# Performance work log

Measured on AMD Instinct MI355X. Metric: run time of the kernel, lower is better.

The kernel has to match this reference:

```python
import jax, jax.numpy as jnp
import numpy as np

B, N, T = 8, 128, 1024
D, LD, H, NQ = 512, 64, 8, 3
HD = D // H
Q = 1 + NQ


def _layernorm(h, g, b):
    m = jnp.mean(h, axis=-1, keepdims=True)
    v = jnp.var(h, axis=-1, keepdims=True)
    return (h - m) * jax.lax.rsqrt(v + 1e-5) * g + b


def setup_inputs() -> dict:
    key = jax.random.key(0)
    ks = jax.random.split(key, 24)
    s = 0.02
    # monotone one-hot alignment: each frame assigned to a sorted phoneme index
    idx = jnp.sort(jax.random.randint(ks[0], (B, T), 0, N), axis=1)
    alignments = jax.nn.one_hot(idx, N, dtype=jnp.float32)  # [B,T,N]
    return dict(
        embeddings=jax.random.normal(ks[1], (B, N, D), jnp.float32),
        alignments=alignments,
        x=jax.random.normal(ks[2], (B, T, D), jnp.float32),
        padding_mask_phoneme=jnp.zeros((B, N), bool),
        padding_mask_frames=jnp.zeros((B, T), bool),
        kl_loss_pooler_weight=jnp.float32(0.01),
        eps=jax.random.normal(ks[3], (B, N, LD), jnp.float32),
        learnable_queries=jax.random.normal(ks[4], (1, 1, NQ, D), jnp.float32),
        in_proj_w=jax.random.normal(ks[5], (3 * D, D), jnp.float32) * s,
        in_proj_b=jnp.zeros((3 * D,), jnp.float32),
        out_proj_w=jax.random.normal(ks[6], (D, D), jnp.float32) * s,
        out_proj_b=jnp.zeros((D,), jnp.float32),
        ln_g=jnp.ones((D,), jnp.float32),
        ln_b=jnp.zeros((D,), jnp.float32),
        bot_w=jax.random.normal(ks[7], (D, Q * D), jnp.float32) * s,
        bot_b=jnp.zeros((D,), jnp.float32),
        mu_w=jax.random.normal(ks[8], (LD, D), jnp.float32) * s,
        mu_b=jnp.zeros((LD,), jnp.float32),
        lv_w=jax.random.normal(ks[9], (LD, D), jnp.float32) * s,
        lv_b=jnp.zeros((LD,), jnp.float32),
        conv1_w=jax.random.normal(ks[10], (D, LD + 1, 3), jnp.float32) * s,
        conv1_b=jnp.zeros((D,), jnp.float32),
        conv2_w=jax.random.normal(ks[11], (D, D, 3), jnp.float32) * s,
        conv2_b=jnp.zeros((D,), jnp.float32),
    )


def reference(embeddings, alignments, x, padding_mask_phoneme, padding_mask_frames,
              kl_loss_pooler_weight, eps, learnable_queries, in_proj_w, in_proj_b,
              out_proj_w, out_proj_b, ln_g, ln_b, bot_w, bot_b, mu_w, mu_b,
              lv_w, lv_b, conv1_w, conv1_b, conv2_w, conv2_b):
    b, n, d = embeddings.shape
    t = x.shape[1]
    # queries: per-phoneme embedding + learnable queries -> [B, N*Q, D]
    q_learn = jnp.broadcast_to(learnable_queries, (b, n, NQ, d))
    queries = jnp.concatenate([embeddings[:, :, None, :], q_learn], axis=2).reshape(b, n * Q, d)
    # data-dependent attention mask from alignments: True = masked
    m = jnp.transpose(alignments, (0, 2, 1))[:, :, None, :]        # [B,N,1,T]
    bool_mask = jnp.broadcast_to(m, (b, n, Q, t)).reshape(b, n * Q, t) == 0
    all_true = jnp.all(bool_mask, axis=-1, keepdims=True)
    bool_mask = jnp.where(all_true, False, bool_mask)
    # multihead cross-attention
    wq, wk, wv = jnp.split(in_proj_w, 3)
    bq, bk, bv = jnp.split(in_proj_b, 3)
    q = (queries @ wq.T + bq).reshape(b, n * Q, H, HD)
    k = (x @ wk.T + bk).reshape(b, t, H, HD)
    v = (x @ wv.T + bv).reshape(b, t, H, HD)
    scores = jnp.einsum('blhd,bshd->bhls', q, k) / jnp.sqrt(jnp.float32(HD))
    scores = jnp.where(bool_mask[:, None, :, :], -jnp.inf, scores)
    attn = jax.nn.softmax(scores, axis=-1)
    ctx = jnp.einsum('bhls,bshd->blhd', attn, v).reshape(b, n * Q, d)
    attn_out = ctx @ out_proj_w.T + out_proj_b
    qn = _layernorm(queries + attn_out, ln_g, ln_b).reshape(b, n, Q * d)
    hidden = jax.nn.silu(qn @ bot_w.T + bot_b)
    # duration-based pooling of x onto phonemes
    dur = jnp.sum(alignments, axis=1)[:, :, None]                  # [B,N,1]
    hidden = hidden + jnp.einsum('btn,btd->bnd', alignments, x) / (dur + 1e-8)
    mu_z = hidden @ mu_w.T + mu_b
    logvar_z = hidden @ lv_w.T + lv_b
    z = mu_z + eps * jnp.exp(0.5 * logvar_z)
    # upsample back to frames + phase feature
    z_up = jnp.einsum('btn,bnl->btl', alignments, z)               # [B,T,LD]
    dur2 = jnp.clip(jnp.sum(alignments, axis=1), 1e-5)             # [B,N]
    running = jnp.cumsum(alignments, axis=1) - 0.5
    phase = jnp.sum((running / dur2[:, None, :]) * alignments, axis=-1, keepdims=True)
    zc = jnp.transpose(jnp.concatenate([z_up, phase], axis=-1), (0, 2, 1))  # [B,LD+1,T]
    dn = ('NCH', 'OIH', 'NCH')
    y = jax.lax.conv_general_dilated(zc, conv1_w, (1,), 'SAME', dimension_numbers=dn) + conv1_b[None, :, None]
    y = jax.nn.silu(y)
    y = jax.lax.conv_general_dilated(y, conv2_w, (1,), 'SAME', dimension_numbers=dn) + conv2_b[None, :, None]
    x_recon = jnp.transpose(y, (0, 2, 1))                          # [B,T,D]
    # losses (masked-select replaced with jit-friendly masked sums)
    valid_p = (~padding_mask_phoneme)[..., None].astype(mu_z.dtype)
    kl = -0.5 * jnp.sum((1.0 + logvar_z - mu_z ** 2 - jnp.exp(logvar_z)) * valid_p)
    kl = kl * jnp.reshape(kl_loss_pooler_weight, ())
    valid_f = (~padding_mask_frames)[..., None].astype(x.dtype)
    diff = (x - x_recon) * valid_f
    cnt = jnp.sum(valid_f) * d
    l1 = jnp.sum(jnp.abs(diff)) / cnt
    l2 = jnp.sum(diff ** 2) / cnt
    return x_recon, kl, l1 + l2
```

## Files before the change

kernel.cpp:

```cpp
#include <hip/hip_runtime.h>
#include <hip/hip_bf16.h>
#include <math.h>

#define B_  8
#define N_  128
#define T_  1024
#define D_  512
#define LD_ 64
#define H_  8
#define Q_  4

typedef __hip_bfloat16 bf16;
typedef __attribute__((ext_vector_type(8))) short short8v;
typedef __attribute__((ext_vector_type(4))) float f32x4;
typedef __attribute__((ext_vector_type(4))) float float4v;
typedef __attribute__((ext_vector_type(4))) unsigned int uint4v;

__device__ __forceinline__ void gload16(const void* g, void* l) {
  __builtin_amdgcn_global_load_lds(
      (const __attribute__((address_space(1))) void*)g,
      (__attribute__((address_space(3))) void*)l, 16, 0, 0);
}

__device__ __forceinline__ void f2b4s(const float* in, bf16* out) {
  float4v v = *(const float4v*)in;
  bf16 o[4] = {bf16(v.x), bf16(v.y), bf16(v.z), bf16(v.w)};
  *(ulong1*)out = *(ulong1*)o;
}

__global__ __launch_bounds__(256) void k_prep(
    const float* __restrict__ x, const float* __restrict__ inw,
    const float* __restrict__ outw, const float* __restrict__ botw,
    const float* __restrict__ c1w, const float* __restrict__ c2w,
    const float* __restrict__ emb, const float* __restrict__ lq,
    bf16* __restrict__ xb, bf16* __restrict__ inwb, bf16* __restrict__ outwb,
    bf16* __restrict__ botwb, bf16* __restrict__ w1tb, bf16* __restrict__ w2tb,
    bf16* __restrict__ qryB,
    int* __restrict__ dur, int* __restrict__ segst, float* __restrict__ lacc)
{
  int g = blockIdx.x * 256 + threadIdx.x;
  if (g < 1048576) {
    f2b4s(x + (size_t)g * 4, xb + (size_t)g * 4);
  } else if (g < 1245184) {
    int i = g - 1048576;
    f2b4s(inw + (size_t)i * 4, inwb + (size_t)i * 4);
  } else if (g < 1310720) {
    int i = g - 1245184;
    f2b4s(outw + (size_t)i * 4, outwb + (size_t)i * 4);
  } else if (g < 1572864) {
    int i = g - 1310720;
    f2b4s(botw + (size_t)i * 4, botwb + (size_t)i * 4);
  } else if (g < 1703936) {
    int i = g - 1572864;
    int kk = i & 255, c = i >> 8;
    float v = 0.f;
    if (kk < 195) { int tap = kk / 65, ii = kk - tap * 65; v = c1w[c * 195 + ii * 3 + tap]; }
    w1tb[i] = bf16(v);
  } else if (g < 2490368) {
    int i = g - 1703936;
    int kk = i % 1536, co = i / 1536;
    int tap = kk >> 9, ci = kk & 511;
    w2tb[i] = bf16(c2w[co * 1536 + ci * 3 + tap]);
  } else if (g < 3014656) {
    int i4 = g - 2490368;
    int e = i4 * 4;
    int d = e & 511;
    int row = e >> 9;
    int j = row & 3;
    int bn = row >> 2;
    const float* src = (j == 0) ? emb + (size_t)bn * 512 + d
                                : lq + (size_t)(j - 1) * 512 + d;
    f2b4s(src, qryB + (size_t)e);
  } else if (g < 3015680) {
    int i = g - 3014656;
    dur[i] = 0; segst[i] = 0x7fffffff;
  } else if (g < 3015682) {
    lacc[g - 3015680] = 0.f;
  }
}

__global__ __launch_bounds__(256) void k_seg_build(
    const float* __restrict__ align, int* __restrict__ idx,
    int* __restrict__ dur, int* __restrict__ segst) {
  int row = blockIdx.x * 4 + (threadIdx.x >> 6);
  int lane = threadIdx.x & 63;
  const float* r = align + (size_t)row * N_;
  unsigned long long m0 = __ballot(r[lane] > 0.5f);
  unsigned long long m1 = __ballot(r[lane + 64] > 0.5f);
  if (lane == 0) {
    int n = m0 ? (__ffsll(m0) - 1) : (m1 ? (__ffsll(m1) - 1 + 64) : 0);
    idx[row] = n;
    int b = row >> 10, t = row & 1023;
    atomicAdd(&dur[b * N_ + n], 1);
    atomicMin(&segst[b * N_ + n], t);
  }
}

template<int EPI, int APAD, int CMODE, typename CT>
__global__ __launch_bounds__(256, 2) void k_mgemm(
    const bf16* __restrict__ A, int lda,
    const bf16* __restrict__ W, int ldw,
    const float* __restrict__ bias,
    CT* __restrict__ C, int ldc,
    int M, int Nc, int K,
    const float* __restrict__ xref = nullptr,
    float* __restrict__ lacc = nullptr)
{
  __shared__ __align__(16) short As[3][4096];
  __shared__ __align__(16) short Bs[3][8192];
  const int tid = threadIdx.x;
  const int m0 = blockIdx.y * 64;
  const int n0 = blockIdx.x * 128;
  const int kbase = blockIdx.z * K;
  const int w = tid >> 6, lane = tid & 63;
  const int wn = w * 32;
  const int lr = lane & 15;
  const int cg = lane >> 4;

  const int rg = lane >> 3;
  const int soff = (((lane & 7) ^ rg) << 3);
  const int rA = w * 8 + rg;
  int gA0 = m0 + rA, gA1 = m0 + rA + 32;
  int ar0 = APAD ? gA0 + ((gA0 >> 10) << 1) : gA0;
  int ar1 = APAD ? gA1 + ((gA1 >> 10) << 1) : gA1;
  const size_t aOff0 = (size_t)ar0 * lda + kbase + soff;
  const size_t aOff1 = (size_t)ar1 * lda + kbase + soff;
  size_t wOffs[4];
#pragma unroll
  for (int j = 0; j < 4; ++j)
    wOffs[j] = (size_t)(n0 + rA + j * 32) * ldw + kbase + soff;

  const int nt = K >> 6;

#define STAGE_(tt, buf) do { \
    size_t kk_ = (size_t)(tt) * 64; \
    gload16(A + aOff0 + kk_, &As[buf][tid * 8]); \
    gload16(A + aOff1 + kk_, &As[buf][2048 + tid * 8]); \
    gload16(W + wOffs[0] + kk_, &Bs[buf][tid * 8]); \
    gload16(W + wOffs[1] + kk_, &Bs[buf][2048 + tid * 8]); \
    gload16(W + wOffs[2] + kk_, &Bs[buf][4096 + tid * 8]); \
    gload16(W + wOffs[3] + kk_, &Bs[buf][6144 + tid * 8]); \
  } while (0)

  STAGE_(0, 0);
  if (nt > 1) STAGE_(1, 1);

  f32x4 acc[4][2] = {};
  int cur = 0;
  for (int t = 0; t < nt; ++t) {
    if (t + 2 < nt) {
      int b2 = cur + 2; if (b2 >= 3) b2 -= 3;
      STAGE_(t + 2, b2);
      asm volatile("s_waitcnt vmcnt(12)" ::: "memory");
    } else if (t + 1 < nt) {
      asm volatile("s_waitcnt vmcnt(6)" ::: "memory");
    } else {
      asm volatile("s_waitcnt vmcnt(0)" ::: "memory");
    }
    __builtin_amdgcn_sched_barrier(0);
    __builtin_amdgcn_s_barrier();
    __builtin_amdgcn_sched_barrier(0);
#pragma unroll
    for (int h = 0; h < 2; ++h) {
      short8v af[4], bfv[2];
#pragma unroll
      for (int i = 0; i < 4; ++i) {
        int rr = i * 16 + lr;
        af[i] = *(const short8v*)&As[cur][rr * 64 + (((h * 4 + cg) ^ (rr & 7)) << 3)];
      }
#pragma unroll
      for (int j = 0; j < 2; ++j) {
        int rr = wn + j * 16 + lr;
        bfv[j] = *(const short8v*)&Bs[cur][rr * 64 + (((h * 4 + cg) ^ (rr & 7)) << 3)];
      }
      __builtin_amdgcn_s_setprio(1);
#pragma unroll
      for (int i = 0; i < 4; ++i)
#pragma unroll
        for (int j = 0; j < 2; ++j)
          acc[i][j] = __builtin_amdgcn_mfma_f32_16x16x32_bf16(af[i], bfv[j], acc[i][j], 0, 0, 0);
      __builtin_amdgcn_s_setprio(0);
    }
    __builtin_amdgcn_sched_barrier(0);
    __builtin_amdgcn_s_barrier();
    __builtin_amdgcn_sched_barrier(0);
    cur = (cur == 2) ? 0 : cur + 1;
  }
#undef STAGE_

  if (EPI == 3) C += (size_t)blockIdx.z * M * ldc;
  const int orow = (lane >> 4) * 4;
  const int ocol = lane & 15;
  float la = 0.f, lb = 0.f;
#pragma unroll
  for (int i = 0; i < 4; ++i) {
#pragma unroll
    for (int q = 0; q < 4; ++q) {
      int gm = m0 + i * 16 + orow + q;
      int cr = CMODE ? gm + ((gm >> 10) << 1) + 1 : gm;
#pragma unroll
      for (int j = 0; j < 2; ++j) {
        int gn = n0 + wn + j * 16 + ocol;
        float v = acc[i][j][q];
        if (EPI != 3) v += bias[gn];
        if (EPI == 1) v = v / (1.f + __expf(-v));
        if (EPI == 4) {
          float diff = xref[(size_t)gm * Nc + gn] - v;
          la += fabsf(diff);
          lb += diff * diff;
        }
        C[(size_t)cr * ldc + gn] = (CT)v;
      }
    }
  }
  if (EPI == 4) {
    __shared__ float sh1[4], sh2[4];
#pragma unroll
    for (int off = 32; off; off >>= 1) { la += __shfl_xor(la, off); lb += __shfl_xor(lb, off); }
    if (lane == 0) { sh1[w] = la; sh2[w] = lb; }
    __syncthreads();
    if (tid == 0) {
      atomicAdd(&lacc[0], sh1[0] + sh1[1] + sh1[2] + sh1[3]);
      atomicAdd(&lacc[1], sh2[0] + sh2[1] + sh2[2] + sh2[3]);
    }
  }
}

__global__ __launch_bounds__(256) void k_attn(
    const bf16* __restrict__ qbuf, const bf16* __restrict__ kv,
    const int* __restrict__ segst, const int* __restrict__ dur,
    bf16* __restrict__ ctx)
{
  int bn = blockIdx.x;
  int b = bn >> 7;
  int w = threadIdx.x >> 6;
  int lane = threadIdx.x & 63;
  int s0 = segst[bn], cnt = dur[bn];
  if (cnt == 0) { s0 = 0; cnt = T_; }
  size_t qrow = (size_t)bn * 4 + w;
  const bf16* kvb = kv + ((size_t)b * T_ + s0) * 1024;

  float qf[8];
  {
    uint4v qv = *(const uint4v*)(qbuf + qrow * 512 + lane * 8);
#pragma unroll
    for (int i = 0; i < 4; ++i) {
      unsigned u = qv[i];
      qf[2 * i]     = __uint_as_float(u << 16);
      qf[2 * i + 1] = __uint_as_float(u & 0xffff0000u);
    }
  }

  float m = -1e30f, l = 0.f;
  float o[8] = {};
  for (int s = 0; s < cnt; s += 4) {
    float sc4[4];
#pragma unroll
    for (int u = 0; u < 4; ++u) {
      int ss = s + u;
      int sscl = (ss < cnt) ? ss : (cnt - 1);
      uint4v kr = *(const uint4v*)(kvb + (size_t)sscl * 1024 + lane * 8);
      float d0 = 0.f;
#pragma unroll
      for (int i = 0; i < 4; ++i) {
        unsigned uu = kr[i];
        d0 = fmaf(qf[2 * i],     __uint_as_float(uu << 16),         d0);
        d0 = fmaf(qf[2 * i + 1], __uint_as_float(uu & 0xffff0000u), d0);
      }
      d0 += __shfl_xor(d0, 1);
      d0 += __shfl_xor(d0, 2);
      d0 += __shfl_xor(d0, 4);
      sc4[u] = (ss < cnt) ? d0 * 0.125f : -1e30f;
    }
    float cmax = fmaxf(fmaxf(sc4[0], sc4[1]), fmaxf(sc4[2], sc4[3]));
    float mn = fmaxf(m, cmax);
    float c = __expf(m - mn);
    float p[4];
#pragma unroll
    for (int u = 0; u < 4; ++u) p[u] = __expf(sc4[u] - mn);
    l = l * c + p[0] + p[1] + p[2] + p[3];
#pragma unroll
    for (int k = 0; k < 8; ++k) o[k] *= c;
#pragma unroll
    for (int u = 0; u < 4; ++u) {
      int ss = s + u;
      int sscl = (ss < cnt) ? ss : (cnt - 1);
      uint4v vr = *(const uint4v*)(kvb + (size_t)sscl * 1024 + 512 + lane * 8);
      float pu = p[u];
#pragma unroll
      for (int i = 0; i < 4; ++i) {
        unsigned uu = vr[i];
        o[2 * i]     = fmaf(pu, __uint_as_float(uu << 16),         o[2 * i]);
        o[2 * i + 1] = fmaf(pu, __uint_as_float(uu & 0xffff0000u), o[2 * i + 1]);
      }
    }
    m = mn;
  }
  float invl = 1.f / l;
  bf16 ob[8];
#pragma unroll
  for (int k = 0; k < 8; ++k) ob[k] = bf16(o[k] * invl);
  *(uint4v*)(ctx + qrow * 512 + lane * 8) = *(uint4v*)ob;
}

__global__ __launch_bounds__(256) void k_lnpool(
    const float* __restrict__ emb, const float* __restrict__ lq,
    const float* __restrict__ attn,
    const float* __restrict__ g, const float* __restrict__ bb,
    bf16* __restrict__ qn,
    const float* __restrict__ x, const int* __restrict__ segst,
    const int* __restrict__ dur, float* __restrict__ pooled)
{
  if (blockIdx.x < 1024) {
    int r = blockIdx.x * 4 + (threadIdx.x >> 6);
    int lane = threadIdx.x & 63;
    int bn = r >> 2, j = r & 3;
    const float* src = (j == 0) ? emb + (size_t)bn * D_ : lq + (size_t)(j - 1) * D_;
    float h[8];
    float s = 0.f, s2 = 0.f;
#pragma unroll
    for (int i = 0; i < 8; ++i) {
      int d = i * 64 + lane;
      float v = src[d] + attn[(size_t)r * D_ + d];
      h[i] = v; s += v; s2 += v * v;
    }
#pragma unroll
    for (int off = 32; off; off >>= 1) { s += __shfl_xor(s, off); s2 += __shfl_xor(s2, off); }
    float mean = s * (1.f / 512.f);
    float var = s2 * (1.f / 512.f) - mean * mean;
    float inv = rsqrtf(var + 1e-5f);
#pragma unroll
    for (int i = 0; i < 8; ++i) {
      int d = i * 64 + lane;
      qn[(size_t)r * D_ + d] = bf16((h[i] - mean) * inv * g[d] + bb[d]);
    }
  } else {
    int bn = blockIdx.x - 1024;
    int b = bn >> 7;
    int s0 = segst[bn], cnt = dur[bn];
    int d0 = threadIdx.x;
    float a0 = 0.f, a1 = 0.f;
    for (int i = 0; i < cnt; ++i) {
      const float* xr = x + (size_t)(b * T_ + s0 + i) * D_;
      a0 += xr[d0];
      a1 += xr[d0 + 256];
    }
    float inv = 1.f / ((float)cnt + 1e-8f);
    pooled[(size_t)bn * D_ + d0] = a0 * inv;
    pooled[(size_t)bn * D_ + d0 + 256] = a1 * inv;
  }
}

__global__ __launch_bounds__(128) void k_muz(
    const float* __restrict__ part, const float* __restrict__ bbias,
    const float* __restrict__ pooled,
    const float* __restrict__ mu_w, const float* __restrict__ mu_b,
    const float* __restrict__ lv_w, const float* __restrict__ lv_b,
    const float* __restrict__ eps, float* __restrict__ z, float* __restrict__ klpart)
{
  __shared__ float hs[512];
  __shared__ float ms[64], ls[64];
  int bn = blockIdx.x;
  int tid = threadIdx.x;
  const size_t S = 1024ull * 512;
  for (int i = tid; i < 512; i += 128) {
    size_t off = (size_t)bn * 512 + i;
    float v = part[off] + part[off + S] + part[off + 2 * S] + part[off + 3 * S] + bbias[i];
    v = v / (1.f + __expf(-v));
    hs[i] = v + pooled[off];
  }
  __syncthreads();
  int ld = tid & 63;
  const float* wrow = (tid < 64) ? (mu_w + (size_t)ld * 512) : (lv_w + (size_t)ld * 512);
  float acc = 0.f;
  for (int k = 0; k < 512; ++k) acc = fmaf(hs[k], wrow[k], acc);
  acc += (tid < 64) ? mu_b[ld] : lv_b[ld];
  if (tid < 64) ms[ld] = acc; else ls[ld] = acc;
  __syncthreads();
  if (tid < 64) {
    float mu = ms[ld], lv = ls[ld];
    z[(size_t)bn * 64 + ld] = mu + eps[(size_t)bn * 64 + ld] * expf(0.5f * lv);
    float klt = 1.f + lv - mu * mu - expf(lv);
#pragma unroll
    for (int off = 32; off; off >>= 1) klt += __shfl_xor(klt, off);
    if (ld == 0) klpart[bn] = klt;
  }
}

__global__ void k_azc(const float* __restrict__ z, const int* __restrict__ idx,
                      const int* __restrict__ segst, const int* __restrict__ dur,
                      bf16* __restrict__ azc, bf16* __restrict__ y1p)
{
  int gid = blockIdx.x * blockDim.x + threadIdx.x;
  if (blockIdx.x < 32) {
    int d = gid & 511;
    int rest = gid >> 9;
    int which = rest & 1;
    int b = rest >> 1;
    int rr = which ? (T_ + 1) : 0;
    y1p[(size_t)(b * (T_ + 2) + rr) * 512 + d] = bf16(0.f);
  }
  if (gid >= 8192 * 256) return;
  int k = gid & 255;
  int m = gid >> 8;
  int b = m >> 10, t = m & 1023;
  float v = 0.f;
  if (k < 195) {
    int tap = k / 65, c = k - tap * 65;
    int tt = t + tap - 1;
    if (tt >= 0 && tt < T_) {
      int iv = idx[b * T_ + tt];
      if (c < 64) v = z[(size_t)(b * N_ + iv) * 64 + c];
      else {
        int s0 = segst[b * N_ + iv];
        float d2 = (float)dur[b * N_ + iv];
        v = ((float)(tt - s0) + 0.5f) / d2;
      }
    }
  }
  azc[gid] = bf16(v);
}

__global__ __launch_bounds__(256) void k_final(
    const float* __restrict__ klpart, const float* __restrict__ lacc,
    const float* __restrict__ klw, float* __restrict__ out)
{
  __shared__ float sa[4];
  float a = 0.f;
  for (int i = threadIdx.x; i < 1024; i += 256) a += klpart[i];
#pragma unroll
  for (int off = 32; off; off >>= 1) a += __shfl_xor(a, off);
  int w = threadIdx.x >> 6, lane = threadIdx.x & 63;
  if (lane == 0) sa[w] = a;
  __syncthreads();
  if (threadIdx.x == 0) {
    float kl = sa[0] + sa[1] + sa[2] + sa[3];
    out[(size_t)B_ * T_ * D_]     = -0.5f * kl * klw[0];
    out[(size_t)B_ * T_ * D_ + 1] = (lacc[0] + lacc[1]) / (float)(B_ * T_ * D_);
  }
}

extern "C" void kernel_launch(void* const* d_in, const int* in_sizes, int n_in,
                              void* d_out, int out_size, void* d_ws, size_t ws_size,
                              hipStream_t stream)
{
  const float* emb  = (const float*)d_in[0];
  const float* algn = (const float*)d_in[1];
  const float* x    = (const float*)d_in[2];
  const float* klw  = (const float*)d_in[5];
  const float* eps  = (const float*)d_in[6];
  const float* lq   = (const float*)d_in[7];
  const float* inw  = (const float*)d_in[8];
  const float* inb  = (const float*)d_in[9];
  const float* outw = (const float*)d_in[10];
  const float* outb = (const float*)d_in[11];
  const float* lng  = (const float*)d_in[12];
  const float* lnb  = (const float*)d_in[13];
  const float* botw = (const float*)d_in[14];
  const float* botb = (const float*)d_in[15];
  const float* muw  = (const float*)d_in[16];
  const float* mub  = (const float*)d_in[17];
  const float* lvw  = (const float*)d_in[18];
  const float* lvb  = (const float*)d_in[19];
  const float* c1w  = (const float*)d_in[20];
  const float* c1b  = (const float*)d_in[21];
  const float* c2w  = (const float*)d_in[22];
  const float* c2b  = (const float*)d_in[23];
  float* out = (float*)d_out;

  float* ws = (float*)d_ws;
  size_t o = 0;
  auto allocF = [&](size_t n) { float* p = ws + o; o += n; return p; };
  auto allocB = [&](size_t n) { bf16* p = (bf16*)(ws + o); o += (n + 1) / 2; return p; };

  bf16* kvB    = allocB(8192ull * 1024);
  bf16* xb     = allocB(8192ull * 512);
  bf16* qryB   = allocB(4096ull * 512);
  bf16* qbufB  = allocB(4096ull * 512);
  bf16* ctxB   = allocB(4096ull * 512);
  bf16* qnB    = allocB(4096ull * 512);
  bf16* inwb   = allocB(1536ull * 512);
  bf16* outwb  = allocB(512ull * 512);
  bf16* botwb  = allocB(512ull * 2048);
  bf16* w1tb   = allocB(512ull * 256);
  bf16* w2tb   = allocB(512ull * 1536);
  bf16* y1p    = allocB(8ull * (T_ + 2) * 512);
  float* attnF  = allocF(4096ull * 512);
  float* pooled = allocF(1024ull * 512);
  float* zbuf   = allocF(1024ull * 64);
  float* klpart = allocF(1024);
  float* lacc   = allocF(2);
  int* idx   = (int*)(ws + o); o += 8192;
  int* segst = (int*)(ws + o); o += 1024;
  int* durI  = (int*)(ws + o); o += 1024;
  bf16* azc  = xb;
  float* botP = attnF;

  k_prep<<<dim3(11781), 256, 0, stream>>>(
      x, inw, outw, botw, c1w, c2w, emb, lq,
      xb, inwb, outwb, botwb, w1tb, w2tb, qryB, durI, segst, lacc);
  k_seg_build<<<dim3(B_ * T_ / 4), 256, 0, stream>>>(algn, idx, durI, segst);

  k_mgemm<0, 0, 0, bf16><<<dim3(8, 128), 256, 0, stream>>>(
      xb, 512, inwb + 512 * 512, 512, inb + 512, kvB, 1024, 8192, 1024, 512);
  k_mgemm<0, 0, 0, bf16><<<dim3(4, 64), 256, 0, stream>>>(
      qryB, 512, inwb, 512, inb, qbufB, 512, 4096, 512, 512);

  k_attn<<<dim3(B_ * N_), 256, 0, stream>>>(qbufB, kvB, segst, durI, ctxB);

  k_mgemm<0, 0, 0, float><<<dim3(4, 64), 256, 0, stream>>>(
      ctxB, 512, outwb, 512, outb, attnF, 512, 4096, 512, 512);

  k_lnpool<<<dim3(2048), 256, 0, stream>>>(
      emb, lq, attnF, lng, lnb, qnB, x, segst, durI, pooled);

  k_mgemm<3, 0, 0, float><<<dim3(4, 16, 4), 256, 0, stream>>>(
      qnB, 2048, botwb, 2048, nullptr, botP, 512, 1024, 512, 512);
  k_muz<<<dim3(B_ * N_), 128, 0, stream>>>(
      botP, botb, pooled, muw, mub, lvw, lvb, eps, zbuf, klpart);

  k_azc<<<dim3(8192 * 256 / 256), 256, 0, stream>>>(zbuf, idx, segst, durI, azc, y1p);

  k_mgemm<1, 0, 1, bf16><<<dim3(4, 128), 256, 0, stream>>>(
      azc, 256, w1tb, 256, c1b, y1p, 512, 8192, 512, 256);
  k_mgemm<4, 1, 0, float><<<dim3(4, 128), 256, 0, stream>>>(
      y1p, 512, w2tb, 1536, c2b, out, 512, 8192, 512, 1536, x, lacc);

  k_final<<<dim3(1), 256, 0, stream>>>(klpart, lacc, klw, out);
}
```

Before: 172.3 us.

## Fuse launches: seg build and pooling into prep, merge KV/Q GEMMs, last-block finalize

Folds segment construction into the prep kernel. Segment starts and durations now come from binary searches over the monotone alignment instead of atomics, and the mean-pooling of x moves into prep as well. The K/V and Q projection GEMMs become a single launch, and the final loss reduction is done by whichever conv2 block finishes last, tracked with a completion counter. The aim is fewer kernel launches and less serialization, at the cost of relying on monotone alignments for the binary search and spending some redundant ballot work.

```diff
diff --git a/kernel.cpp b/kernel.cpp
--- a/kernel.cpp
+++ b/kernel.cpp
@@ -6,9 +6,6 @@
 #define N_  128
 #define T_  1024
 #define D_  512
-#define LD_ 64
-#define H_  8
-#define Q_  4
 
 typedef __hip_bfloat16 bf16;
 typedef __attribute__((ext_vector_type(8))) short short8v;
@@ -28,90 +25,129 @@
   *(ulong1*)out = *(ulong1*)o;
 }
 
+__device__ __forceinline__ int eval_idx(const float* __restrict__ algn,
+                                        int b, int t, int lane) {
+  const float* r = algn + ((size_t)b * T_ + t) * N_;
+  unsigned long long m0 = __ballot(r[lane] > 0.5f);
+  unsigned long long m1 = __ballot(r[lane + 64] > 0.5f);
+  return m0 ? (__ffsll(m0) - 1) : (m1 ? (__ffsll(m1) - 1 + 64) : 0);
+}
+__device__ __forceinline__ int lower_bound_t(const float* __restrict__ algn,
+                                             int b, int n, int lane) {
+  int lo = 0, hi = 1024;
+  while (lo < hi) {
+    int mid = (lo + hi) >> 1;
+    if (eval_idx(algn, b, mid, lane) >= n) hi = mid; else lo = mid + 1;
+  }
+  return lo;
+}
+
 __global__ __launch_bounds__(256) void k_prep(
     const float* __restrict__ x, const float* __restrict__ inw,
     const float* __restrict__ outw, const float* __restrict__ botw,
     const float* __restrict__ c1w, const float* __restrict__ c2w,
     const float* __restrict__ emb, const float* __restrict__ lq,
+    const float* __restrict__ algn,
     bf16* __restrict__ xb, bf16* __restrict__ inwb, bf16* __restrict__ outwb,
     bf16* __restrict__ botwb, bf16* __restrict__ w1tb, bf16* __restrict__ w2tb,
-    bf16* __restrict__ qryB,
-    int* __restrict__ dur, int* __restrict__ segst, float* __restrict__ lacc)
-{
-  int g = blockIdx.x * 256 + threadIdx.x;
-  if (g < 1048576) {
-    f2b4s(x + (size_t)g * 4, xb + (size_t)g * 4);
-  } else if (g < 1245184) {
-    int i = g - 1048576;
-    f2b4s(inw + (size_t)i * 4, inwb + (size_t)i * 4);
-  } else if (g < 1310720) {
-    int i = g - 1245184;
-    f2b4s(outw + (size_t)i * 4, outwb + (size_t)i * 4);
-  } else if (g < 1572864) {
-    int i = g - 1310720;
-    f2b4s(botw + (size_t)i * 4, botwb + (size_t)i * 4);
-  } else if (g < 1703936) {
-    int i = g - 1572864;
-    int kk = i & 255, c = i >> 8;
-    float v = 0.f;
-    if (kk < 195) { int tap = kk / 65, ii = kk - tap * 65; v = c1w[c * 195 + ii * 3 + tap]; }
-    w1tb[i] = bf16(v);
-  } else if (g < 2490368) {
-    int i = g - 1703936;
-    int kk = i % 1536, co = i / 1536;
-    int tap = kk >> 9, ci = kk & 511;
-    w2tb[i] = bf16(c2w[co * 1536 + ci * 3 + tap]);
-  } else if (g < 3014656) {
-    int i4 = g - 2490368;
-    int e = i4 * 4;
-    int d = e & 511;
-    int row = e >> 9;
-    int j = row & 3;
-    int bn = row >> 2;
-    const float* src = (j == 0) ? emb + (size_t)bn * 512 + d
-                                : lq + (size_t)(j - 1) * 512 + d;
-    f2b4s(src, qryB + (size_t)e);
-  } else if (g < 3015680) {
-    int i = g - 3014656;
-    dur[i] = 0; segst[i] = 0x7fffffff;
-  } else if (g < 3015682) {
-    lacc[g - 3015680] = 0.f;
-  }
-}
-
-__global__ __launch_bounds__(256) void k_seg_build(
-    const float* __restrict__ align, int* __restrict__ idx,
-    int* __restrict__ dur, int* __restrict__ segst) {
-  int row = blockIdx.x * 4 + (threadIdx.x >> 6);
-  int lane = threadIdx.x & 63;
-  const float* r = align + (size_t)row * N_;
-  unsigned long long m0 = __ballot(r[lane] > 0.5f);
-  unsigned long long m1 = __ballot(r[lane + 64] > 0.5f);
-  if (lane == 0) {
-    int n = m0 ? (__ffsll(m0) - 1) : (m1 ? (__ffsll(m1) - 1 + 64) : 0);
-    idx[row] = n;
+    bf16* __restrict__ qryB, int* __restrict__ idx,
+    int* __restrict__ dur, int* __restrict__ segst,
+    float* __restrict__ lacc, int* __restrict__ donecnt,
+    float* __restrict__ pooled)
+{
+  const int bid = blockIdx.x;
+  const int tid = threadIdx.x;
+  const int lane = tid & 63;
+  const int w = tid >> 6;
+  if (bid < 11777) {
+    int g = bid * 256 + tid;
+    if (g < 1048576) {
+      f2b4s(x + (size_t)g * 4, xb + (size_t)g * 4);
+    } else if (g < 1245184) {
+      int i = g - 1048576;
+      f2b4s(inw + (size_t)i * 4, inwb + (size_t)i * 4);
+    } else if (g < 1310720) {
+      int i = g - 1245184;
+      f2b4s(outw + (size_t)i * 4, outwb + (size_t)i * 4);
+    } else if (g < 1572864) {
+      int i = g - 1310720;
+      f2b4s(botw + (size_t)i * 4, botwb + (size_t)i * 4);
+    } else if (g < 1703936) {
+      int i = g - 1572864;
+      int kk = i & 255, c = i >> 8;
+      float v = 0.f;
+      if (kk < 195) { int tap = kk / 65, ii = kk - tap * 65; v = c1w[c * 195 + ii * 3 + tap]; }
+      w1tb[i] = bf16(v);
+    } else if (g < 2490368) {
+      int i = g - 1703936;
+      int kk = i % 1536, co = i / 1536;
+      int tap = kk >> 9, ci = kk & 511;
+      w2tb[i] = bf16(c2w[co * 1536 + ci * 3 + tap]);
+    } else if (g < 3014656) {
+      int i4 = g - 2490368;
+      int e = i4 * 4;
+      int d = e & 511;
+      int row = e >> 9;
+      int j = row & 3;
+      int bn = row >> 2;
+      const float* src = (j == 0) ? emb + (size_t)bn * 512 + d
+                                  : lq + (size_t)(j - 1) * 512 + d;
+      f2b4s(src, qryB + (size_t)e);
+    } else if (g < 3014668) {
+      int i = g - 3014656;
+      if (i < 2) lacc[i] = 0.f;
+      else if (i == 2) *donecnt = 0;
+    }
+  } else if (bid < 13825) {
+    int row = (bid - 11777) * 4 + w;
     int b = row >> 10, t = row & 1023;
-    atomicAdd(&dur[b * N_ + n], 1);
-    atomicMin(&segst[b * N_ + n], t);
+    int n = eval_idx(algn, b, t, lane);
+    if (lane == 0) idx[row] = n;
+  } else if (bid < 14081) {
+    int wid = (bid - 13825) * 4 + w;
+    int b = wid >> 7, n = wid & 127;
+    int l1 = lower_bound_t(algn, b, n, lane);
+    int l2 = lower_bound_t(algn, b, n + 1, lane);
+    if (lane == 0) { segst[wid] = l1; dur[wid] = l2 - l1; }
+  } else {
+    __shared__ int sseg[2];
+    int bn = bid - 14081;
+    int b = bn >> 7, n = bn & 127;
+    if (w == 0) {
+      int l1 = lower_bound_t(algn, b, n, lane);
+      int l2 = lower_bound_t(algn, b, n + 1, lane);
+      if (lane == 0) { sseg[0] = l1; sseg[1] = l2 - l1; }
+    }
+    __syncthreads();
+    int s0 = sseg[0], cnt = sseg[1];
+    int d0 = tid;
+    float a0 = 0.f, a1 = 0.f;
+    for (int i = 0; i < cnt; ++i) {
+      const float* xr = x + (size_t)(b * T_ + s0 + i) * D_;
+      a0 += xr[d0];
+      a1 += xr[d0 + 256];
+    }
+    float inv = 1.f / ((float)cnt + 1e-8f);
+    pooled[(size_t)bn * D_ + d0] = a0 * inv;
+    pooled[(size_t)bn * D_ + d0 + 256] = a1 * inv;
   }
 }
 
 template<int EPI, int APAD, int CMODE, typename CT>
-__global__ __launch_bounds__(256, 2) void k_mgemm(
+__device__ __forceinline__ void mgemm_body(
     const bf16* __restrict__ A, int lda,
     const bf16* __restrict__ W, int ldw,
     const float* __restrict__ bias,
     CT* __restrict__ C, int ldc,
-    int M, int Nc, int K,
-    const float* __restrict__ xref = nullptr,
-    float* __restrict__ lacc = nullptr)
+    int M, int Nc, int K, int bx, int by, int bz,
+    const float* __restrict__ xref, float* __restrict__ lacc)
 {
   __shared__ __align__(16) short As[3][4096];
   __shared__ __align__(16) short Bs[3][8192];
   const int tid = threadIdx.x;
-  const int m0 = blockIdx.y * 64;
-  const int n0 = blockIdx.x * 128;
-  const int kbase = blockIdx.z * K;
+  const int m0 = by * 64;
+  const int n0 = bx * 128;
+  const int kbase = bz * K;
   const int w = tid >> 6, lane = tid & 63;
   const int wn = w * 32;
   const int lr = lane & 15;
@@ -188,7 +224,7 @@
   }
 #undef STAGE_
 
-  if (EPI == 3) C += (size_t)blockIdx.z * M * ldc;
+  if (EPI == 3) C += (size_t)bz * M * ldc;
   const int orow = (lane >> 4) * 4;
   const int ocol = lane & 15;
   float la = 0.f, lb = 0.f;
@@ -226,6 +262,88 @@
   }
 }
 
+__global__ __launch_bounds__(256, 2) void k_kvq(
+    const bf16* __restrict__ xb, const bf16* __restrict__ qryB,
+    const bf16* __restrict__ inwb, const float* __restrict__ inb,
+    bf16* __restrict__ kvB, bf16* __restrict__ qbufB)
+{
+  int bid = blockIdx.x;
+  const bf16 *A, *W; const float* bias; bf16* C;
+  int ldc, M, Nc, bx, by;
+  if (bid < 1024) {
+    A = xb; W = inwb + 512 * 512; bias = inb + 512; C = kvB;
+    ldc = 1024; M = 8192; Nc = 1024; bx = bid & 7; by = bid >> 3;
+  } else {
+    int i = bid - 1024;
+    A = qryB; W = inwb; bias = inb; C = qbufB;
+    ldc = 512; M = 4096; Nc = 512; bx = i & 3; by = i >> 2;
+  }
+  mgemm_body<0, 0, 0, bf16>(A, 512, W, 512, bias, C, ldc, M, Nc, 512,
+                            bx, by, 0, nullptr, nullptr);
+}
+
+__global__ __launch_bounds__(256, 2) void k_outp(
+    const bf16* __restrict__ ctxB, const bf16* __restrict__ outwb,
+    const float* __restrict__ outb, float* __restrict__ attnF)
+{
+  mgemm_body<0, 0, 0, float>(ctxB, 512, outwb, 512, outb, attnF, 512,
+                             4096, 512, 512, blockIdx.x, blockIdx.y, 0,
+                             nullptr, nullptr);
+}
+
+__global__ __launch_bounds__(256, 2) void k_bot(
+    const bf16* __restrict__ qnB, const bf16* __restrict__ botwb,
+    float* __restrict__ botP)
+{
+  mgemm_body<3, 0, 0, float>(qnB, 2048, botwb, 2048, nullptr, botP, 512,
+                             1024, 512, 512, blockIdx.x, blockIdx.y, blockIdx.z,
+                             nullptr, nullptr);
+}
+
+__global__ __launch_bounds__(256, 2) void k_conv1(
+    const bf16* __restrict__ azc, const bf16* __restrict__ w1tb,
+    const float* __restrict__ c1b, bf16* __restrict__ y1p)
+{
+  mgemm_body<1, 0, 1, bf16>(azc, 256, w1tb, 256, c1b, y1p, 512,
+                            8192, 512, 256, blockIdx.x, blockIdx.y, 0,
+                            nullptr, nullptr);
+}
+
+__global__ __launch_bounds__(256, 2) void k_conv2(
+    const bf16* __restrict__ y1p, const bf16* __restrict__ w2tb,
+    const float* __restrict__ c2b, float* __restrict__ out,
+    const float* __restrict__ x, float* __restrict__ lacc,
+    const float* __restrict__ klpart, const float* __restrict__ klw,
+    int* __restrict__ donecnt)
+{
+  mgemm_body<4, 1, 0, float>(y1p, 512, w2tb, 1536, c2b, out, 512,
+                             8192, 512, 1536, blockIdx.x, blockIdx.y, 0,
+                             x, lacc);
+  __shared__ int lastFlag;
+  __threadfence();
+  if (threadIdx.x == 0) {
+    int old = atomicAdd(donecnt, 1);
+    lastFlag = (old == 4 * 128 - 1);
+  }
+  __syncthreads();
+  if (lastFlag) {
+    int tid = threadIdx.x, lane = tid & 63, w = tid >> 6;
+    float a = klpart[tid] + klpart[tid + 256] + klpart[tid + 512] + klpart[tid + 768];
+#pragma unroll
+    for (int off = 32; off; off >>= 1) a += __shfl_xor(a, off);
+    __shared__ float sa[4];
+    if (lane == 0) sa[w] = a;
+    __syncthreads();
+    if (tid == 0) {
+      float kl = sa[0] + sa[1] + sa[2] + sa[3];
+      float l1 = atomicAdd(&lacc[0], 0.f);
+      float l2 = atomicAdd(&lacc[1], 0.f);
+      out[(size_t)B_ * T_ * D_]     = -0.5f * kl * klw[0];
+      out[(size_t)B_ * T_ * D_ + 1] = (l1 + l2) / (float)(B_ * T_ * D_);
+    }
+  }
+}
+
 __global__ __launch_bounds__(256) void k_attn(
     const bf16* __restrict__ qbuf, const bf16* __restrict__ kv,
     const int* __restrict__ segst, const int* __restrict__ dur,
@@ -303,51 +421,33 @@
   *(uint4v*)(ctx + qrow * 512 + lane * 8) = *(uint4v*)ob;
 }
 
-__global__ __launch_bounds__(256) void k_lnpool(
+__global__ __launch_bounds__(256) void k_ln(
     const float* __restrict__ emb, const float* __restrict__ lq,
     const float* __restrict__ attn,
     const float* __restrict__ g, const float* __restrict__ bb,
-    bf16* __restrict__ qn,
-    const float* __restrict__ x, const int* __restrict__ segst,
-    const int* __restrict__ dur, float* __restrict__ pooled)
-{
-  if (blockIdx.x < 1024) {
-    int r = blockIdx.x * 4 + (threadIdx.x >> 6);
-    int lane = threadIdx.x & 63;
-    int bn = r >> 2, j = r & 3;
-    const float* src = (j == 0) ? emb + (size_t)bn * D_ : lq + (size_t)(j - 1) * D_;
-    float h[8];
-    float s = 0.f, s2 = 0.f;
-#pragma unroll
-    for (int i = 0; i < 8; ++i) {
-      int d = i * 64 + lane;
-      float v = src[d] + attn[(size_t)r * D_ + d];
-      h[i] = v; s += v; s2 += v * v;
-    }
-#pragma unroll
-    for (int off = 32; off; off >>= 1) { s += __shfl_xor(s, off); s2 += __shfl_xor(s2, off); }
-    float mean = s * (1.f / 512.f);
-    float var = s2 * (1.f / 512.f) - mean * mean;
-    float inv = rsqrtf(var + 1e-5f);
-#pragma unroll
-    for (int i = 0; i < 8; ++i) {
-      int d = i * 64 + lane;
-      qn[(size_t)r * D_ + d] = bf16((h[i] - mean) * inv * g[d] + bb[d]);
-    }
-  } else {
-    int bn = blockIdx.x - 1024;
-    int b = bn >> 7;
-    int s0 = segst[bn], cnt = dur[bn];
-    int d0 = threadIdx.x;
-    float a0 = 0.f, a1 = 0.f;
-    for (int i = 0; i < cnt; ++i) {
-      const float* xr = x + (size_t)(b * T_ + s0 + i) * D_;
-      a0 += xr[d0];
-      a1 += xr[d0 + 256];
-    }
-    float inv = 1.f / ((float)cnt + 1e-8f);
-    pooled[(size_t)bn * D_ + d0] = a0 * inv;
-    pooled[(size_t)bn * D_ + d0 + 256] = a1 * inv;
+    bf16* __restrict__ qn)
+{
+  int r = blockIdx.x * 4 + (threadIdx.x >> 6);
+  int lane = threadIdx.x & 63;
+  int bn = r >> 2, j = r & 3;
+  const float* src = (j == 0) ? emb + (size_t)bn * D_ : lq + (size_t)(j - 1) * D_;
+  float h[8];
+  float s = 0.f, s2 = 0.f;
+#pragma unroll
+  for (int i = 0; i < 8; ++i) {
+    int d = i * 64 + lane;
+    float v = src[d] + attn[(size_t)r * D_ + d];
+    h[i] = v; s += v; s2 += v * v;
+  }
+#pragma unroll
+  for (int off = 32; off; off >>= 1) { s += __shfl_xor(s, off); s2 += __shfl_xor(s2, off); }
+  float mean = s * (1.f / 512.f);
+  float var = s2 * (1.f / 512.f) - mean * mean;
+  float inv = rsqrtf(var + 1e-5f);
+#pragma unroll
+  for (int i = 0; i < 8; ++i) {
+    int d = i * 64 + lane;
+    qn[(size_t)r * D_ + d] = bf16((h[i] - mean) * inv * g[d] + bb[d]);
   }
 }
 
@@ -419,25 +519,6 @@
     }
   }
   azc[gid] = bf16(v);
-}
-
-__global__ __launch_bounds__(256) void k_final(
-    const float* __restrict__ klpart, const float* __restrict__ lacc,
-    const float* __restrict__ klw, float* __restrict__ out)
-{
-  __shared__ float sa[4];
-  float a = 0.f;
-  for (int i = threadIdx.x; i < 1024; i += 256) a += klpart[i];
-#pragma unroll
-  for (int off = 32; off; off >>= 1) a += __shfl_xor(a, off);
-  int w = threadIdx.x >> 6, lane = threadIdx.x & 63;
-  if (lane == 0) sa[w] = a;
-  __syncthreads();
-  if (threadIdx.x == 0) {
-    float kl = sa[0] + sa[1] + sa[2] + sa[3];
-    out[(size_t)B_ * T_ * D_]     = -0.5f * kl * klw[0];
-    out[(size_t)B_ * T_ * D_ + 1] = (lacc[0] + lacc[1]) / (float)(B_ * T_ * D_);
-  }
 }
 
 extern "C" void kernel_launch(void* const* d_in, const int* in_sizes, int n_in,
@@ -490,41 +571,35 @@
   float* zbuf   = allocF(1024ull * 64);
   float* klpart = allocF(1024);
   float* lacc   = allocF(2);
+  int* donecnt = (int*)(ws + o); o += 16;
   int* idx   = (int*)(ws + o); o += 8192;
   int* segst = (int*)(ws + o); o += 1024;
   int* durI  = (int*)(ws + o); o += 1024;
   bf16* azc  = xb;
   float* botP = attnF;
 
-  k_prep<<<dim3(11781), 256, 0, stream>>>(
-      x, inw, outw, botw, c1w, c2w, emb, lq,
-      xb, inwb, outwb, botwb, w1tb, w2tb, qryB, durI, segst, lacc);
-  k_seg_build<<<dim3(B_ * T_ / 4), 256, 0, stream>>>(algn, idx, durI, segst);
-
-  k_mgemm<0, 0, 0, bf16><<<dim3(8, 128), 256, 0, stream>>>(
-      xb, 512, inwb + 512 * 512, 512, inb + 512, kvB, 1024, 8192, 1024, 512);
-  k_mgemm<0, 0, 0, bf16><<<dim3(4, 64), 256, 0, stream>>>(
-      qryB, 512, inwb, 512, inb, qbufB, 512, 4096, 512, 512);
+  k_prep<<<dim3(15105), 256, 0, stream>>>(
+      x, inw, outw, botw, c1w, c2w, emb, lq, algn,
+      xb, inwb, outwb, botwb, w1tb, w2tb, qryB, idx, durI, segst,
+      lacc, donecnt, pooled);
+
+  k_kvq<<<dim3(1280), 256, 0, stream>>>(xb, qryB, inwb, inb, kvB, qbufB);
 
   k_attn<<<dim3(B_ * N_), 256, 0, stream>>>(qbufB, kvB, segst, durI, ctxB);
 
-  k_mgemm<0, 0, 0, float><<<dim3(4, 64), 256, 0, stream>>>(
-      ctxB, 512, outwb, 512, outb, attnF, 512, 4096, 512, 512);
-
-  k_lnpool<<<dim3(2048), 256, 0, stream>>>(
-      emb, lq, attnF, lng, lnb, qnB, x, segst, durI, pooled);
-
-  k_mgemm<3, 0, 0, float><<<dim3(4, 16, 4), 256, 0, stream>>>(
-      qnB, 2048, botwb, 2048, nullptr, botP, 512, 1024, 512, 512);
+  k_outp<<<dim3(4, 64), 256, 0, stream>>>(ctxB, outwb, outb, attnF);
+
+  k_ln<<<dim3(1024), 256, 0, stream>>>(emb, lq, attnF, lng, lnb, qnB);
+
+  k_bot<<<dim3(4, 16, 4), 256, 0, stream>>>(qnB, botwb, botP);
+
   k_muz<<<dim3(B_ * N_), 128, 0, stream>>>(
       botP, botb, pooled, muw, mub, lvw, lvb, eps, zbuf, klpart);
 
   k_azc<<<dim3(8192 * 256 / 256), 256, 0, stream>>>(zbuf, idx, segst, durI, azc, y1p);
 
-  k_mgemm<1, 0, 1, bf16><<<dim3(4, 128), 256, 0, stream>>>(
-      azc, 256, w1tb, 256, c1b, y1p, 512, 8192, 512, 256);
-  k_mgemm<4, 1, 0, float><<<dim3(4, 128), 256, 0, stream>>>(
-      y1p, 512, w2tb, 1536, c2b, out, 512, 8192, 512, 1536, x, lacc);
-
-  k_final<<<dim3(1), 256, 0, stream>>>(klpart, lacc, klw, out);
-}
+  k_conv1<<<dim3(4, 128), 256, 0, stream>>>(azc, w1tb, c1b, y1p);
+
+  k_conv2<<<dim3(4, 128), 256, 0, stream>>>(
+      y1p, w2tb, c2b, out, x, lacc, klpart, klw, donecnt);
+}
```

New measurement: 223.3 us. +29.6%, slower.
